# Performance work log

Hardware: AMD Instinct MI355X
Metric: run time of the kernel (lower is better)

The kernel has to match this reference:

```python
import jax, jax.numpy as jnp
import numpy as np

H, D = 16, 64  # num_heads, head_dim (hidden = H*D = 1024)
EPS = 1e-6

def elu_plus_one(x):
    return jax.nn.elu(x) + 1.0

def setup_inputs() -> dict:
    key = jax.random.key(0)
    ks = jax.random.split(key, 12)
    hid = H * D
    s = 0.02
    return {
        "hidden_states": jax.random.normal(ks[0], (1, 2048, hid), jnp.float32),
        "w_q": jax.random.normal(ks[1], (hid, hid), jnp.float32) * s,
        "w_k": jax.random.normal(ks[2], (hid, hid), jnp.float32) * s,
        "w_v": jax.random.normal(ks[3], (hid, hid), jnp.float32) * s,
        "w_o": jax.random.normal(ks[4], (hid, hid), jnp.float32) * s,
        "memory_gate": jnp.zeros((H,), jnp.float32),
        "eg_w1": jax.random.normal(ks[5], (hid, hid // 4), jnp.float32) * s,
        "eg_b1": jnp.zeros((hid // 4,), jnp.float32),
        "eg_w2": jax.random.normal(ks[6], (hid // 4, 1), jnp.float32) * s,
        "eg_b2": jnp.zeros((1,), jnp.float32),
        "fine_mem": jax.random.normal(ks[7], (4, H, D, D), jnp.float32) * s,
        "fine_norm": jax.random.uniform(ks[8], (4, H, D), jnp.float32),
    }

def _retrieve(sigma_q, memory, memory_norm):
    # sigma_q: [b,h,s,d], memory: [h,d,e], memory_norm: [h,d]
    a = jnp.einsum('bhsd,hde->bhse', sigma_q, memory)
    relevance = jnp.einsum('bhsd,hd->bhs', sigma_q, memory_norm)
    out = a / jnp.clip(relevance, EPS, None)[..., None]
    return out, relevance

def reference(hidden_states, w_q, w_k, w_v, w_o, memory_gate,
              eg_w1, eg_b1, eg_w2, eg_b2, fine_mem, fine_norm):
    B, S, hid = hidden_states.shape
    def proj(w):
        return (hidden_states @ w).reshape(B, S, H, D).transpose(0, 2, 1, 3)  # [b,h,s,d]
    q, k, v = proj(w_q), proj(w_k), proj(w_v)
    sigma_q = elu_plus_one(q)

    # coarse memory = sum of fine memories
    M_coarse = fine_mem.sum(0)        # [h,d,d]
    z_coarse = fine_norm.sum(0)       # [h,d]
    output_coarse, _ = _retrieve(sigma_q, M_coarse, z_coarse)  # [b,h,s,d]

    # learned expansion gate on coarse representation
    coarse_repr = output_coarse.transpose(0, 2, 1, 3).reshape(B, S, hid)
    logit = jax.nn.relu(coarse_repr @ eg_w1 + eg_b1) @ eg_w2 + eg_b2  # [b,s,1]
    expansion_prob = jax.nn.sigmoid(logit)                            # [b,s,1]

    # fine-grained retrieval: attention-weighted mix over the 4 banks
    outs = jnp.einsum('bhsd,fhde->fbhse', sigma_q, fine_mem)   # [f,b,h,s,d]
    rels = jnp.einsum('bhsd,fhd->fbhs', sigma_q, fine_norm)    # [f,b,h,s]
    outs = outs / jnp.clip(rels, EPS, None)[..., None]
    weights = jax.nn.softmax(rels.mean(-1), axis=0)            # [f,b,h]
    output_fine = (outs * weights[:, :, :, None, None]).sum(0)  # [b,h,s,d]

    ep = expansion_prob.transpose(0, 2, 1)[..., None]          # [b,1,s,1]
    memory_output = ep * output_fine + (1.0 - ep) * output_coarse

    # causal linear attention within current segment
    sigma_k = elu_plus_one(k)
    kv = jnp.einsum('bhsd,bhse->bhsde', sigma_k, v)            # [b,h,s,d,d]
    kv_cumsum = jnp.cumsum(kv, axis=2)
    k_cumsum = jnp.cumsum(sigma_k, axis=2)
    num = jnp.einsum('bhsd,bhsde->bhse', sigma_q, kv_cumsum)
    den = jnp.clip(jnp.einsum('bhsd,bhsd->bhs', sigma_q, k_cumsum), EPS, None)[..., None]
    local_output = num / den

    gate = jax.nn.sigmoid(memory_gate).reshape(1, H, 1, 1)
    output = gate * memory_output + (1.0 - gate) * local_output
    output = output.transpose(0, 2, 1, 3).reshape(B, S, hid)
    return output @ w_o
```

## Files before the change

### kernel.cpp

```cpp
#include <hip/hip_runtime.h>
#include <cmath>

#define EPSF 1e-6f
#define LDK 72


typedef __attribute__((ext_vector_type(8))) short bf16x8;
typedef __attribute__((ext_vector_type(4))) float f32x4;
typedef __attribute__((ext_vector_type(8))) unsigned short u16x8;

__device__ __forceinline__ float wave_allsum(float v) {
#pragma unroll
  for (int off = 32; off > 0; off >>= 1) v += __shfl_xor(v, off, 64);
  return v;
}

__device__ __forceinline__ unsigned short f2bf(float f) {
  unsigned int u = __float_as_uint(f);
  unsigned int r = (u + 0x7fffu + ((u >> 16) & 1u)) >> 16;
  return (unsigned short)r;
}
__device__ __forceinline__ float bf2f(unsigned short u) {
  return __uint_as_float(((unsigned int)u) << 16);
}

__global__ __launch_bounds__(256) void prep_kernel(const float* __restrict__ FM,
    const float* __restrict__ FN, const float* __restrict__ HS,
    const float* __restrict__ W0, const float* __restrict__ W1,
    const float* __restrict__ W2, const float* __restrict__ W3,
    const float* __restrict__ EGW1,
    unsigned short* __restrict__ MCT, float* __restrict__ ZC,
    unsigned short* __restrict__ T0, unsigned short* __restrict__ T1,
    unsigned short* __restrict__ T2, unsigned short* __restrict__ T3,
    unsigned short* __restrict__ W1T, unsigned short* __restrict__ FMT,
    unsigned short* __restrict__ HSB)
{
  int b = blockIdx.x, tid = threadIdx.x;
  __shared__ float tile[64][65];
  if (b < 64) {
    int h = b >> 2, q = b & 3;
    for (int i = tid; i < 1024; i += 256) {
      int dpl = i >> 6, e = i & 63;
      int idx = (q * 16 + dpl) * 64 + e;
      tile[dpl][e] = FM[(0 * 16 + h) * 4096 + idx] + FM[(1 * 16 + h) * 4096 + idx]
                   + FM[(2 * 16 + h) * 4096 + idx] + FM[(3 * 16 + h) * 4096 + idx];
    }
    if (q == 0 && tid < 64)
      ZC[h * 64 + tid] = FN[h * 64 + tid] + FN[1024 + h * 64 + tid]
                       + FN[2048 + h * 64 + tid] + FN[3072 + h * 64 + tid];
    __syncthreads();
    for (int i = tid; i < 1024; i += 256) {
      int e = i >> 4, dpl = i & 15;
      MCT[h * 4096 + e * 64 + q * 16 + dpl] = f2bf(tile[dpl][e]);
    }
  } else if (b < 1088) {
    int r0 = b - 64, z = r0 >> 8, rem = r0 & 255;
    const float* W = (z == 0) ? W0 : (z == 1) ? W1 : (z == 2) ? W2 : W3;
    unsigned short* WT = (z == 0) ? T0 : (z == 1) ? T1 : (z == 2) ? T2 : T3;
    int n0 = (rem & 15) * 64, k0 = (rem >> 4) * 64;
    for (int i = tid; i < 4096; i += 256) {
      int r = i >> 6, c = i & 63;
      tile[r][c] = W[(k0 + r) * 1024 + n0 + c];
    }
    __syncthreads();
    for (int i = tid; i < 1024; i += 256) {
      int r = i >> 4, c4 = (i & 15) * 4;
      ushort4 o;
      o.x = f2bf(tile[c4 + 0][r]); o.y = f2bf(tile[c4 + 1][r]);
      o.z = f2bf(tile[c4 + 2][r]); o.w = f2bf(tile[c4 + 3][r]);
      *reinterpret_cast<ushort4*>(&WT[(n0 + r) * 1024 + k0 + c4]) = o;
    }
  } else if (b < 1152) {
    int rem = b - 1088;
    int n0 = (rem & 3) * 64, k0 = (rem >> 2) * 64;
    for (int i = tid; i < 4096; i += 256) {
      int r = i >> 6, c = i & 63;
      tile[r][c] = EGW1[(k0 + r) * 256 + n0 + c];
    }
    __syncthreads();
    for (int i = tid; i < 1024; i += 256) {
      int r = i >> 4, c4 = (i & 15) * 4;
      ushort4 o;
      o.x = f2bf(tile[c4 + 0][r]); o.y = f2bf(tile[c4 + 1][r]);
      o.z = f2bf(tile[c4 + 2][r]); o.w = f2bf(tile[c4 + 3][r]);
      *reinterpret_cast<ushort4*>(&W1T[(n0 + r) * 1024 + k0 + c4]) = o;
    }
  } else if (b < 1216) {
    int mat = b - 1152;
    const float* src = FM + mat * 4096;
    for (int i = tid; i < 4096; i += 256) tile[i >> 6][i & 63] = src[i];
    __syncthreads();
    unsigned short* dst = FMT + mat * 4096;
    for (int i = tid; i < 4096; i += 256) {
      int e = i >> 6, dp = i & 63;
      dst[e * 64 + dp] = f2bf(tile[dp][e]);
    }
  } else {
    int i = (b - 1216) * 256 + tid;
    float4 v = *reinterpret_cast<const float4*>(HS + i * 4);
    ushort4 o; o.x = f2bf(v.x); o.y = f2bf(v.y); o.z = f2bf(v.z); o.w = f2bf(v.w);
    *reinterpret_cast<ushort4*>(HSB + i * 4) = o;
  }
}

__global__ __launch_bounds__(256) void mm_bf16(const unsigned short* __restrict__ A,
    const unsigned short* __restrict__ BT, float* __restrict__ C, int ldc, int act)
{
  __shared__ unsigned short As[128 * LDK];
  __shared__ unsigned short Bs[128 * LDK];
  int tid = threadIdx.x;
  int m0 = blockIdx.y * 128, n0 = blockIdx.x * 128;
  int wid = tid >> 6, lane = tid & 63;
  int wr = wid >> 1, wc = wid & 1;
  int lr = lane & 15, lg = lane >> 4;

  f32x4 acc[4][4];
#pragma unroll
  for (int m = 0; m < 4; ++m)
#pragma unroll
    for (int n = 0; n < 4; ++n)
#pragma unroll
      for (int r = 0; r < 4; ++r) acc[m][n][r] = 0.f;

  for (int kt = 0; kt < 16; ++kt) {
    int k0 = kt * 64;
#pragma unroll
    for (int p = 0; p < 4; ++p) {
      int c = p * 256 + tid;
      int row = c >> 3, k8 = c & 7;
      u16x8 va = *reinterpret_cast<const u16x8*>(A + (m0 + row) * 1024 + k0 + k8 * 8);
      *reinterpret_cast<u16x8*>(&As[row * LDK + k8 * 8]) = va;
      u16x8 vb = *reinterpret_cast<const u16x8*>(BT + (n0 + row) * 1024 + k0 + k8 * 8);
      *reinterpret_cast<u16x8*>(&Bs[row * LDK + k8 * 8]) = vb;
    }
    __syncthreads();
#pragma unroll
    for (int kk = 0; kk < 2; ++kk) {
      bf16x8 af[4], bfr[4];
#pragma unroll
      for (int m = 0; m < 4; ++m)
        af[m] = *reinterpret_cast<const bf16x8*>(&As[(wr * 64 + m * 16 + lr) * LDK + kk * 32 + lg * 8]);
#pragma unroll
      for (int n = 0; n < 4; ++n)
        bfr[n] = *reinterpret_cast<const bf16x8*>(&Bs[(wc * 64 + n * 16 + lr) * LDK + kk * 32 + lg * 8]);
#pragma unroll
      for (int m = 0; m < 4; ++m)
#pragma unroll
        for (int n = 0; n < 4; ++n)
          acc[m][n] = __builtin_amdgcn_mfma_f32_16x16x32_bf16(af[m], bfr[n], acc[m][n], 0, 0, 0);
    }
    __syncthreads();
  }
#pragma unroll
  for (int m = 0; m < 4; ++m)
#pragma unroll
    for (int n = 0; n < 4; ++n)
#pragma unroll
      for (int r = 0; r < 4; ++r) {
        float v = acc[m][n][r];
        if (act) v = v > 0.f ? v + 1.f : expf(v);
        C[(m0 + wr * 64 + m * 16 + lg * 4 + r) * ldc + n0 + wc * 64 + n * 16 + lr] = v;
      }
}

__global__ __launch_bounds__(256) void mm_gate_bf16(const unsigned short* __restrict__ MOB,
    const unsigned short* __restrict__ LOB, const float* __restrict__ MG,
    const unsigned short* __restrict__ BT, float* __restrict__ C)
{
  __shared__ unsigned short As[128 * LDK];
  __shared__ unsigned short Bs[128 * LDK];
  __shared__ float gs[16];
  int tid = threadIdx.x;
  int m0 = blockIdx.y * 128, n0 = blockIdx.x * 128;
  int wid = tid >> 6, lane = tid & 63;
  int wr = wid >> 1, wc = wid & 1;
  int lr = lane & 15, lg = lane >> 4;
  if (tid < 16) gs[tid] = 1.f / (1.f + expf(-MG[tid]));
  __syncthreads();

  f32x4 acc[4][4];
#pragma unroll
  for (int m = 0; m < 4; ++m)
#pragma unroll
    for (int n = 0; n < 4; ++n)
#pragma unroll
      for (int r = 0; r < 4; ++r) acc[m][n][r] = 0.f;

  for (int kt = 0; kt < 16; ++kt) {
    int k0 = kt * 64;
#pragma unroll
    for (int p = 0; p < 4; ++p) {
      int c = p * 256 + tid;
      int row = c >> 3, k8 = c & 7;
      int col = k0 + k8 * 8;
      float g = gs[col >> 6];
      u16x8 mv = *reinterpret_cast<const u16x8*>(MOB + (m0 + row) * 1024 + col);
      u16x8 lv = *reinterpret_cast<const u16x8*>(LOB + (m0 + row) * 1024 + col);
      u16x8 o;
#pragma unroll
      for (int j = 0; j < 8; ++j)
        o[j] = f2bf(g * bf2f((unsigned short)mv[j]) + (1.f - g) * bf2f((unsigned short)lv[j]));
      *reinterpret_cast<u16x8*>(&As[row * LDK + k8 * 8]) = o;
      u16x8 vb = *reinterpret_cast<const u16x8*>(BT + (n0 + row) * 1024 + k0 + k8 * 8);
      *reinterpret_cast<u16x8*>(&Bs[row * LDK + k8 * 8]) = vb;
    }
    __syncthreads();
#pragma unroll
    for (int kk = 0; kk < 2; ++kk) {
      bf16x8 af[4], bfr[4];
#pragma unroll
      for (int m = 0; m < 4; ++m)
        af[m] = *reinterpret_cast<const bf16x8*>(&As[(wr * 64 + m * 16 + lr) * LDK + kk * 32 + lg * 8]);
#pragma unroll
      for (int n = 0; n < 4; ++n)
        bfr[n] = *reinterpret_cast<const bf16x8*>(&Bs[(wc * 64 + n * 16 + lr) * LDK + kk * 32 + lg * 8]);
#pragma unroll
      for (int m = 0; m < 4; ++m)
#pragma unroll
        for (int n = 0; n < 4; ++n)
          acc[m][n] = __builtin_amdgcn_mfma_f32_16x16x32_bf16(af[m], bfr[n], acc[m][n], 0, 0, 0);
    }
    __syncthreads();
  }
#pragma unroll
  for (int m = 0; m < 4; ++m)
#pragma unroll
    for (int n = 0; n < 4; ++n)
#pragma unroll
      for (int r = 0; r < 4; ++r)
        C[(m0 + wr * 64 + m * 16 + lg * 4 + r) * 1024 + n0 + wc * 64 + n * 16 + lr] = acc[m][n][r];
}

__global__ __launch_bounds__(256) void proj_bf16(const unsigned short* __restrict__ A,
    const unsigned short* __restrict__ WqT, const unsigned short* __restrict__ WkT,
    const unsigned short* __restrict__ WvT,
    unsigned short* __restrict__ Oq, unsigned short* __restrict__ Ok,
    unsigned short* __restrict__ Ov)
{
  int z = blockIdx.z;
  const unsigned short* BT = (z == 0) ? WqT : (z == 1) ? WkT : WvT;
  unsigned short* C = (z == 0) ? Oq : (z == 1) ? Ok : Ov;

  __shared__ unsigned short As[128 * LDK];
  __shared__ unsigned short Bs[128 * LDK];
  int tid = threadIdx.x;
  int m0 = blockIdx.y * 128, n0 = blockIdx.x * 128;
  int wid = tid >> 6, lane = tid & 63;
  int wr = wid >> 1, wc = wid & 1;
  int lr = lane & 15, lg = lane >> 4;
  int act = (z < 2) ? 1 : 0;

  f32x4 acc[4][4];
#pragma unroll
  for (int m = 0; m < 4; ++m)
#pragma unroll
    for (int n = 0; n < 4; ++n)
#pragma unroll
      for (int r = 0; r < 4; ++r) acc[m][n][r] = 0.f;

  for (int kt = 0; kt < 16; ++kt) {
    int k0 = kt * 64;
#pragma unroll
    for (int p = 0; p < 4; ++p) {
      int c = p * 256 + tid;
      int row = c >> 3, k8 = c & 7;
      u16x8 va = *reinterpret_cast<const u16x8*>(A + (m0 + row) * 1024 + k0 + k8 * 8);
      *reinterpret_cast<u16x8*>(&As[row * LDK + k8 * 8]) = va;
      u16x8 vb = *reinterpret_cast<const u16x8*>(BT + (n0 + row) * 1024 + k0 + k8 * 8);
      *reinterpret_cast<u16x8*>(&Bs[row * LDK + k8 * 8]) = vb;
    }
    __syncthreads();
#pragma unroll
    for (int kk = 0; kk < 2; ++kk) {
      bf16x8 af[4], bfr[4];
#pragma unroll
      for (int m = 0; m < 4; ++m)
        af[m] = *reinterpret_cast<const bf16x8*>(&As[(wr * 64 + m * 16 + lr) * LDK + kk * 32 + lg * 8]);
#pragma unroll
      for (int n = 0; n < 4; ++n)
        bfr[n] = *reinterpret_cast<const bf16x8*>(&Bs[(wc * 64 + n * 16 + lr) * LDK + kk * 32 + lg * 8]);
#pragma unroll
      for (int m = 0; m < 4; ++m)
#pragma unroll
        for (int n = 0; n < 4; ++n)
          acc[m][n] = __builtin_amdgcn_mfma_f32_16x16x32_bf16(af[m], bfr[n], acc[m][n], 0, 0, 0);
    }
    __syncthreads();
  }
#pragma unroll
  for (int m = 0; m < 4; ++m)
#pragma unroll
    for (int n = 0; n < 4; ++n)
#pragma unroll
      for (int r = 0; r < 4; ++r) {
        float v = acc[m][n][r];
        if (act) v = v > 0.f ? v + 1.f : expf(v);
        C[(m0 + wr * 64 + m * 16 + lg * 4 + r) * 1024 + n0 + wc * 64 + n * 16 + lr] = f2bf(v);
      }
}

__global__ __launch_bounds__(256) void eg_fin(const float* __restrict__ H1,
    const float* __restrict__ B1, const float* __restrict__ W2,
    const float* __restrict__ B2, float* __restrict__ EP)
{
  int wid = threadIdx.x >> 6, lane = threadIdx.x & 63;
  int s = blockIdx.x * 4 + wid;
  float4 h = *reinterpret_cast<const float4*>(H1 + s * 256 + lane * 4);
  float4 b = *reinterpret_cast<const float4*>(B1 + lane * 4);
  float4 w = *reinterpret_cast<const float4*>(W2 + lane * 4);
  float v = fmaxf(h.x + b.x, 0.f) * w.x + fmaxf(h.y + b.y, 0.f) * w.y
          + fmaxf(h.z + b.z, 0.f) * w.z + fmaxf(h.w + b.w, 0.f) * w.w;
  v = wave_allsum(v);
  if (lane == 0) EP[s] = 1.f / (1.f + expf(-(v + B2[0])));
}

__global__ __launch_bounds__(256) void rels_kernel(const unsigned short* __restrict__ SQB,
    const float* __restrict__ ZC, const float* __restrict__ FN,
    float* __restrict__ RELC, float* __restrict__ RELS, float* __restrict__ PARTS)
{
  int h = blockIdx.x, st = blockIdx.y, tid = threadIdx.x;
  int s0 = st * 64;
  __shared__ float sqT[64][68];
  __shared__ float zf[5][64];
  __shared__ float relb[5][64];
#pragma unroll
  for (int p = 0; p < 2; ++p) {
    int cidx = p * 256 + tid;
    int r = cidx >> 3, d8 = cidx & 7;
    u16x8 v = *reinterpret_cast<const u16x8*>(SQB + (s0 + r) * 1024 + h * 64 + d8 * 8);
#pragma unroll
    for (int j = 0; j < 8; ++j) sqT[d8 * 8 + j][r] = bf2f((unsigned short)v[j]);
  }
  for (int idx = tid; idx < 320; idx += 256) {
    int w = idx >> 6, d = idx & 63;
    zf[w][d] = (w == 0) ? ZC[h * 64 + d] : FN[(w - 1) * 1024 + h * 64 + d];
  }
  __syncthreads();
  {
    int s = tid & 63, wh = tid >> 6;
    float r = 0.f;
    for (int dp = 0; dp < 64; ++dp) r += sqT[dp][s] * zf[wh][dp];
    relb[wh][s] = r;
    if (wh == 0) {
      float r4 = 0.f;
      for (int dp = 0; dp < 64; ++dp) r4 += sqT[dp][s] * zf[4][dp];
      relb[4][s] = r4;
    }
  }
  __syncthreads();
  if (tid < 64) {
    RELC[h * 2048 + s0 + tid] = relb[0][tid];
#pragma unroll
    for (int f = 0; f < 4; ++f)
      RELS[f * 32768 + h * 2048 + s0 + tid] = relb[1 + f][tid];
#pragma unroll
    for (int f = 0; f < 4; ++f) {
      float v = wave_allsum(relb[1 + f][tid]);
      if (tid == 0) PARTS[f * 512 + h * 32 + st] = v;
    }
  }
}

__global__ __launch_bounds__(256) void coarse_mfma(const unsigned short* __restrict__ SQB,
    const unsigned short* __restrict__ MCT, const float* __restrict__ RELC,
    unsigned short* __restrict__ COB)
{
  int h = blockIdx.x, st = blockIdx.y, tid = threadIdx.x;
  int w = tid >> 6, lane = tid & 63, lr = lane & 15, lg = lane >> 4;
  int s0 = st * 128;
  __shared__ unsigned short A_lds[128 * LDK];
  __shared__ unsigned short B_lds[64 * LDK];
#pragma unroll
  for (int p = 0; p < 4; ++p) {
    int c = p * 256 + tid;
    int row = c >> 3, k8 = c & 7;
    *reinterpret_cast<u16x8*>(&A_lds[row * LDK + k8 * 8]) =
        *reinterpret_cast<const u16x8*>(SQB + (s0 + row) * 1024 + h * 64 + k8 * 8);
  }
#pragma unroll
  for (int p = 0; p < 2; ++p) {
    int c = p * 256 + tid;
    int e = c >> 3, k8 = c & 7;
    *reinterpret_cast<u16x8*>(&B_lds[e * LDK + k8 * 8]) =
        *reinterpret_cast<const u16x8*>(MCT + h * 4096 + e * 64 + k8 * 8);
  }
  __syncthreads();

  f32x4 acc[2][4];
#pragma unroll
  for (int m = 0; m < 2; ++m)
#pragma unroll
    for (int n = 0; n < 4; ++n)
#pragma unroll
      for (int r = 0; r < 4; ++r) acc[m][n][r] = 0.f;

#pragma unroll
  for (int kk = 0; kk < 2; ++kk) {
    bf16x8 af[2], bfr[4];
#pragma unroll
    for (int m = 0; m < 2; ++m)
      af[m] = *reinterpret_cast<const bf16x8*>(&A_lds[(w * 32 + m * 16 + lr) * LDK + kk * 32 + lg * 8]);
#pragma unroll
    for (int n = 0; n < 4; ++n)
      bfr[n] = *reinterpret_cast<const bf16x8*>(&B_lds[(n * 16 + lr) * LDK + kk * 32 + lg * 8]);
#pragma unroll
    for (int m = 0; m < 2; ++m)
#pragma unroll
      for (int n = 0; n < 4; ++n)
        acc[m][n] = __builtin_amdgcn_mfma_f32_16x16x32_bf16(af[m], bfr[n], acc[m][n], 0, 0, 0);
  }
#pragma unroll
  for (int m = 0; m < 2; ++m)
#pragma unroll
    for (int r = 0; r < 4; ++r) {
      int s = s0 + w * 32 + m * 16 + lg * 4 + r;
      float rc = fmaxf(RELC[h * 2048 + s], EPSF);
#pragma unroll
      for (int n = 0; n < 4; ++n)
        COB[s * 1024 + h * 64 + n * 16 + lr] = f2bf(acc[m][n][r] / rc);
    }
}

__global__ __launch_bounds__(256) void fine_mfma(const unsigned short* __restrict__ SQB,
    const unsigned short* __restrict__ FMT, const float* __restrict__ RELS,
    const float* __restrict__ PARTS, const float* __restrict__ EP,
    const unsigned short* __restrict__ COB, unsigned short* __restrict__ MOB)
{
  int h = blockIdx.x, st = blockIdx.y;
  int tid = threadIdx.x;
  int w = tid >> 6, lane = tid & 63;
  int lr = lane & 15, lg = lane >> 4;
  int s0 = st * 128;

  __shared__ unsigned short A_lds[128 * LDK];
  __shared__ unsigned short B_lds[4 * 64 * LDK];
  __shared__ float rmean[4];
  if (tid < 4) {
    float s = 0.f;
    for (int t = 0; t < 32; ++t) s += PARTS[tid * 512 + h * 32 + t];
    rmean[tid] = s * (1.f / 2048.f);
  }

#pragma unroll
  for (int p = 0; p < 4; ++p) {
    int c = p * 256 + tid;
    int row = c >> 3, k8 = c & 7;
    *reinterpret_cast<u16x8*>(&A_lds[row * LDK + k8 * 8]) =
        *reinterpret_cast<const u16x8*>(SQB + (s0 + row) * 1024 + h * 64 + k8 * 8);
  }
#pragma unroll
  for (int p = 0; p < 8; ++p) {
    int c = p * 256 + tid;
    int f = c >> 9, rem = c & 511;
    int e = rem >> 3, k8 = rem & 7;
    *reinterpret_cast<u16x8*>(&B_lds[(f * 64 + e) * LDK + k8 * 8]) =
        *reinterpret_cast<const u16x8*>(FMT + (f * 16 + h) * 4096 + e * 64 + k8 * 8);
  }
  __syncthreads();

  f32x4 acc[4][2][4];
#pragma unroll
  for (int f = 0; f < 4; ++f)
#pragma unroll
    for (int m = 0; m < 2; ++m)
#pragma unroll
      for (int n = 0; n < 4; ++n)
#pragma unroll
        for (int r = 0; r < 4; ++r) acc[f][m][n][r] = 0.f;

#pragma unroll
  for (int kk = 0; kk < 2; ++kk) {
    bf16x8 af[2];
#pragma unroll
    for (int m = 0; m < 2; ++m)
      af[m] = *reinterpret_cast<const bf16x8*>(&A_lds[(w * 32 + m * 16 + lr) * LDK + kk * 32 + lg * 8]);
#pragma unroll
    for (int f = 0; f < 4; ++f) {
      bf16x8 bf4[4];
#pragma unroll
      for (int n = 0; n < 4; ++n)
        bf4[n] = *reinterpret_cast<const bf16x8*>(&B_lds[(f * 64 + n * 16 + lr) * LDK + kk * 32 + lg * 8]);
#pragma unroll
      for (int m = 0; m < 2; ++m)
#pragma unroll
        for (int n = 0; n < 4; ++n)
          acc[f][m][n] = __builtin_amdgcn_mfma_f32_16x16x32_bf16(af[m], bf4[n], acc[f][m][n], 0, 0, 0);
    }
  }

  float rm = fmaxf(fmaxf(rmean[0], rmean[1]), fmaxf(rmean[2], rmean[3]));
  float e0 = expf(rmean[0] - rm), e1 = expf(rmean[1] - rm);
  float e2 = expf(rmean[2] - rm), e3 = expf(rmean[3] - rm);
  float winv = 1.f / (e0 + e1 + e2 + e3);
  float w0 = e0 * winv, w1 = e1 * winv, w2 = e2 * winv, w3 = e3 * winv;

#pragma unroll
  for (int m = 0; m < 2; ++m)
#pragma unroll
    for (int r = 0; r < 4; ++r) {
      int s = s0 + w * 32 + m * 16 + lg * 4 + r;
      float e = EP[s];
      float i0 = w0 / fmaxf(RELS[0 * 32768 + h * 2048 + s], EPSF);
      float i1 = w1 / fmaxf(RELS[1 * 32768 + h * 2048 + s], EPSF);
      float i2 = w2 / fmaxf(RELS[2 * 32768 + h * 2048 + s], EPSF);
      float i3 = w3 / fmaxf(RELS[3 * 32768 + h * 2048 + s], EPSF);
#pragma unroll
      for (int n = 0; n < 4; ++n) {
        int dg = h * 64 + n * 16 + lr;
        float fine = acc[0][m][n][r] * i0 + acc[1][m][n][r] * i1
                   + acc[2][m][n][r] * i2 + acc[3][m][n][r] * i3;
        float cv = bf2f(COB[s * 1024 + dg]);
        MOB[s * 1024 + dg] = f2bf(e * fine + (1.f - e) * cv);
      }
    }
}

__global__ __launch_bounds__(256) void chunk_mfma(const unsigned short* __restrict__ SKB,
    const unsigned short* __restrict__ VVB, float* __restrict__ ST)
{
  int h = blockIdx.x, c = blockIdx.y, tid = threadIdx.x;
  int w = tid >> 6, lane = tid & 63, lr = lane & 15, lg = lane >> 4;
  int sb = c * 64;
  __shared__ unsigned short A_lds[64 * LDK];
  __shared__ unsigned short B_lds[80 * LDK];
#pragma unroll
  for (int p = 0; p < 2; ++p) {
    int cc = p * 256 + tid;
    int t = cc >> 3, e8 = cc & 7;
    u16x8 kv = *reinterpret_cast<const u16x8*>(SKB + (sb + t) * 1024 + h * 64 + e8 * 8);
    u16x8 vv = *reinterpret_cast<const u16x8*>(VVB + (sb + t) * 1024 + h * 64 + e8 * 8);
#pragma unroll
    for (int j = 0; j < 8; ++j) {
      A_lds[(e8 * 8 + j) * LDK + t] = (unsigned short)kv[j];
      B_lds[(e8 * 8 + j) * LDK + t] = (unsigned short)vv[j];
    }
  }
  if (tid < 64) B_lds[64 * LDK + tid] = 0x3F80;
  for (int i = tid; i < 15 * 64; i += 256) {
    int row = 65 + (i >> 6), col = i & 63;
    B_lds[row * LDK + col] = 0;
  }
  __syncthreads();

  f32x4 acc[5];
#pragma unroll
  for (int n = 0; n < 5; ++n)
#pragma unroll
    for (int r = 0; r < 4; ++r) acc[n][r] = 0.f;
#pragma unroll
  for (int kk = 0; kk < 2; ++kk) {
    bf16x8 af = *reinterpret_cast<const bf16x8*>(&A_lds[(w * 16 + lr) * LDK + kk * 32 + lg * 8]);
#pragma unroll
    for (int n = 0; n < 5; ++n) {
      bf16x8 bfr = *reinterpret_cast<const bf16x8*>(&B_lds[(n * 16 + lr) * LDK + kk * 32 + lg * 8]);
      acc[n] = __builtin_amdgcn_mfma_f32_16x16x32_bf16(af, bfr, acc[n], 0, 0, 0);
    }
  }
  float* base = ST + (h * 32 + c) * 4160;
#pragma unroll
  for (int r = 0; r < 4; ++r) {
    int d = w * 16 + lg * 4 + r;
#pragma unroll
    for (int n = 0; n < 4; ++n)
      base[d * 64 + n * 16 + lr] = acc[n][r];
    if (lr == 0) base[4096 + d] = acc[4][r];
  }
}

__global__ __launch_bounds__(256) void scan_kernel(const float* __restrict__ ST,
    unsigned short* __restrict__ STB)
{
  int gidx = blockIdx.x * 256 + threadIdx.x;
  int h = gidx / 4160, idx = gidx - h * 4160;
  if (h >= 16) return;
  float run = 0.f;
#pragma unroll 4
  for (int c = 0; c < 32; ++c) {
    float t = ST[(h * 32 + c) * 4160 + idx];
    STB[(h * 32 + c) * 4160 + idx] = f2bf(run);
    run += t;
  }
}

__global__ __launch_bounds__(256) void lattn_mfma(const unsigned short* __restrict__ SQB,
    const unsigned short* __restrict__ SKB, const unsigned short* __restrict__ VVB,
    const unsigned short* __restrict__ STB, unsigned short* __restrict__ LOB)
{
  int h = blockIdx.x, c = blockIdx.y, tid = threadIdx.x;
  int w = tid >> 6, lane = tid & 63, lr = lane & 15, lg = lane >> 4;
  int sb = c * 64;
  const unsigned short* stb = STB + (h * 32 + c) * 4160;

  __shared__ unsigned short A_lds[64 * LDK];
  __shared__ unsigned short K_lds[64 * LDK];
  __shared__ unsigned short P_lds[80 * LDK];
  __shared__ unsigned short V_lds[80 * LDK];
  __shared__ unsigned short S_lds[64 * LDK];

#pragma unroll
  for (int p = 0; p < 2; ++p) {
    int cc = p * 256 + tid;
    int row = cc >> 3, k8 = cc & 7;
    *reinterpret_cast<u16x8*>(&A_lds[row * LDK + k8 * 8]) =
        *reinterpret_cast<const u16x8*>(SQB + (sb + row) * 1024 + h * 64 + k8 * 8);
    *reinterpret_cast<u16x8*>(&K_lds[row * LDK + k8 * 8]) =
        *reinterpret_cast<const u16x8*>(SKB + (sb + row) * 1024 + h * 64 + k8 * 8);
  }
  for (int i = tid; i < 4096; i += 256) {
    int d = i >> 6, e = i & 63;
    P_lds[e * LDK + d] = stb[i];
  }
#pragma unroll
  for (int p = 0; p < 2; ++p) {
    int cc = p * 256 + tid;
    int t = cc >> 3, e8 = cc & 7;
    u16x8 v = *reinterpret_cast<const u16x8*>(VVB + (sb + t) * 1024 + h * 64 + e8 * 8);
#pragma unroll
    for (int j = 0; j < 8; ++j) V_lds[(e8 * 8 + j) * LDK + t] = (unsigned short)v[j];
  }
  if (tid < 64) {
    P_lds[64 * LDK + tid] = stb[4096 + tid];
    V_lds[64 * LDK + tid] = 0x3F80;
  }
  for (int i = tid; i < 15 * 64; i += 256) {
    int row = 65 + (i >> 6), col = i & 63;
    P_lds[row * LDK + col] = 0;
    V_lds[row * LDK + col] = 0;
  }
  __syncthreads();

  f32x4 acc_i[5];
#pragma unroll
  for (int n = 0; n < 5; ++n)
#pragma unroll
    for (int r = 0; r < 4; ++r) acc_i[n][r] = 0.f;
#pragma unroll
  for (int kk = 0; kk < 2; ++kk) {
    bf16x8 af = *reinterpret_cast<const bf16x8*>(&A_lds[(w * 16 + lr) * LDK + kk * 32 + lg * 8]);
#pragma unroll
    for (int n = 0; n < 5; ++n) {
      bf16x8 bfr = *reinterpret_cast<const bf16x8*>(&P_lds[(n * 16 + lr) * LDK + kk * 32 + lg * 8]);
      acc_i[n] = __builtin_amdgcn_mfma_f32_16x16x32_bf16(af, bfr, acc_i[n], 0, 0, 0);
    }
  }
  f32x4 acc_s[4];
#pragma unroll
  for (int n = 0; n < 4; ++n)
#pragma unroll
    for (int r = 0; r < 4; ++r) acc_s[n][r] = 0.f;
#pragma unroll
  for (int kk = 0; kk < 2; ++kk) {
    bf16x8 af = *reinterpret_cast<const bf16x8*>(&A_lds[(w * 16 + lr) * LDK + kk * 32 + lg * 8]);
#pragma unroll
    for (int n = 0; n < 4; ++n) {
      bf16x8 bfr = *reinterpret_cast<const bf16x8*>(&K_lds[(n * 16 + lr) * LDK + kk * 32 + lg * 8]);
      acc_s[n] = __builtin_amdgcn_mfma_f32_16x16x32_bf16(af, bfr, acc_s[n], 0, 0, 0);
    }
  }
#pragma unroll
  for (int n = 0; n < 4; ++n)
#pragma unroll
    for (int r = 0; r < 4; ++r) {
      int s_loc = w * 16 + lg * 4 + r, t = n * 16 + lr;
      float v = (t <= s_loc) ? acc_s[n][r] : 0.f;
      S_lds[s_loc * LDK + t] = f2bf(v);
    }
  __syncthreads();
  f32x4 acc_p[5];
#pragma unroll
  for (int n = 0; n < 5; ++n)
#pragma unroll
    for (int r = 0; r < 4; ++r) acc_p[n][r] = 0.f;
#pragma unroll
  for (int kk = 0; kk < 2; ++kk) {
    bf16x8 af = *reinterpret_cast<const bf16x8*>(&S_lds[(w * 16 + lr) * LDK + kk * 32 + lg * 8]);
#pragma unroll
    for (int n = 0; n < 5; ++n) {
      bf16x8 bfr = *reinterpret_cast<const bf16x8*>(&V_lds[(n * 16 + lr) * LDK + kk * 32 + lg * 8]);
      acc_p[n] = __builtin_amdgcn_mfma_f32_16x16x32_bf16(af, bfr, acc_p[n], 0, 0, 0);
    }
  }
#pragma unroll
  for (int r = 0; r < 4; ++r) {
    float den = acc_i[4][r] + acc_p[4][r];
    den = __shfl(den, lane & 48);
    den = fmaxf(den, EPSF);
    int s = sb + w * 16 + lg * 4 + r;
#pragma unroll
    for (int n = 0; n < 4; ++n)
      LOB[s * 1024 + h * 64 + n * 16 + lr] = f2bf((acc_i[n][r] + acc_p[n][r]) / den);
  }
}

extern "C" void kernel_launch(void* const* d_in, const int* in_sizes, int n_in,
                              void* d_out, int out_size, void* d_ws, size_t ws_size,
                              hipStream_t stream)
{
  const float* hs   = (const float*)d_in[0];
  const float* wq   = (const float*)d_in[1];
  const float* wk   = (const float*)d_in[2];
  const float* wv   = (const float*)d_in[3];
  const float* wo   = (const float*)d_in[4];
  const float* mg   = (const float*)d_in[5];
  const float* egw1 = (const float*)d_in[6];
  const float* egb1 = (const float*)d_in[7];
  const float* egw2 = (const float*)d_in[8];
  const float* egb2 = (const float*)d_in[9];
  const float* fm   = (const float*)d_in[10];
  const float* fn   = (const float*)d_in[11];
  float* out = (float*)d_out;

  float* ws     = (float*)d_ws;
  float* zc     = ws;
  float* rels   = zc + 1024;
  float* parts  = rels + 131072;
  float* ep     = parts + 2048;
  float* relc   = ep + 2048;
  float* states = relc + 32768;
  float* h1     = states + 2129920;
  unsigned short* hsb  = (unsigned short*)(h1 + 524288);
  unsigned short* sqb  = hsb + 2097152;
  unsigned short* skb  = sqb + 2097152;
  unsigned short* vvb  = skb + 2097152;
  unsigned short* cob  = vvb + 2097152;
  unsigned short* mob  = cob + 2097152;
  unsigned short* lob  = mob + 2097152;
  unsigned short* wqT  = lob + 2097152;
  unsigned short* wkT  = wqT + 1048576;
  unsigned short* wvT  = wkT + 1048576;
  unsigned short* woT  = wvT + 1048576;
  unsigned short* w1T  = woT + 1048576;
  unsigned short* fmbT = w1T + 262144;
  unsigned short* mcT  = fmbT + 262144;
  unsigned short* statesb = mcT + 65536;

  prep_kernel<<<3264, 256, 0, stream>>>(fm, fn, hs, wq, wk, wv, wo, egw1,
      mcT, zc, wqT, wkT, wvT, woT, w1T, fmbT, hsb);
  proj_bf16<<<dim3(8, 16, 3), 256, 0, stream>>>(hsb, wqT, wkT, wvT, sqb, skb, vvb);
  rels_kernel<<<dim3(16, 32), 256, 0, stream>>>(sqb, zc, fn, relc, rels, parts);
  coarse_mfma<<<dim3(16, 16), 256, 0, stream>>>(sqb, mcT, relc, cob);
  mm_bf16<<<dim3(2, 16), 256, 0, stream>>>(cob, w1T, h1, 256, 0);
  eg_fin<<<512, 256, 0, stream>>>(h1, egb1, egw2, egb2, ep);
  fine_mfma<<<dim3(16, 16), 256, 0, stream>>>(sqb, fmbT, rels, parts, ep, cob, mob);
  chunk_mfma<<<dim3(16, 32), 256, 0, stream>>>(skb, vvb, states);
  scan_kernel<<<260, 256, 0, stream>>>(states, statesb);
  lattn_mfma<<<dim3(16, 32), 256, 0, stream>>>(sqb, skb, vvb, statesb, lob);
  mm_gate_bf16<<<dim3(8, 16), 256, 0, stream>>>(mob, lob, mg, woT, out);
}
```

Baseline: 127.2 us.

## Merge independent memory and linear-attention stages into combined horizontal-fusion launches

Independent stages that used to be separate launches now share kernels, with the work chosen by block index: relevance with chunk states, coarse retrieval with the state scan, and local attention with the gate's first GEMM. This cuts the launch count from 11 to 8 and lets small, under-filled grids run side by side on the device. In exchange, the fused kernels reserve the larger of the two shared-memory footprints, which may lower occupancy, and blocks of different cost now run in the same grid.

```diff
diff --git a/kernel.cpp b/kernel.cpp
--- a/kernel.cpp
+++ b/kernel.cpp
@@ -103,9 +103,16 @@
   }
 }
 
-__global__ __launch_bounds__(256) void mm_bf16(const unsigned short* __restrict__ A,
-    const unsigned short* __restrict__ BT, float* __restrict__ C, int ldc, int act)
-{
+__global__ __launch_bounds__(256) void proj_bf16(const unsigned short* __restrict__ A,
+    const unsigned short* __restrict__ WqT, const unsigned short* __restrict__ WkT,
+    const unsigned short* __restrict__ WvT,
+    unsigned short* __restrict__ Oq, unsigned short* __restrict__ Ok,
+    unsigned short* __restrict__ Ov)
+{
+  int z = blockIdx.z;
+  const unsigned short* BT = (z == 0) ? WqT : (z == 1) ? WkT : WvT;
+  unsigned short* C = (z == 0) ? Oq : (z == 1) ? Ok : Ov;
+
   __shared__ unsigned short As[128 * LDK];
   __shared__ unsigned short Bs[128 * LDK];
   int tid = threadIdx.x;
@@ -113,6 +120,7 @@
   int wid = tid >> 6, lane = tid & 63;
   int wr = wid >> 1, wc = wid & 1;
   int lr = lane & 15, lg = lane >> 4;
+  int act = (z < 2) ? 1 : 0;
 
   f32x4 acc[4][4];
 #pragma unroll
@@ -159,8 +167,463 @@
       for (int r = 0; r < 4; ++r) {
         float v = acc[m][n][r];
         if (act) v = v > 0.f ? v + 1.f : expf(v);
-        C[(m0 + wr * 64 + m * 16 + lg * 4 + r) * ldc + n0 + wc * 64 + n * 16 + lr] = v;
-      }
+        C[(m0 + wr * 64 + m * 16 + lg * 4 + r) * 1024 + n0 + wc * 64 + n * 16 + lr] = f2bf(v);
+      }
+}
+
+__global__ __launch_bounds__(256) void mid1_kernel(const unsigned short* __restrict__ SQB,
+    const float* __restrict__ ZC, const float* __restrict__ FN,
+    const unsigned short* __restrict__ SKB, const unsigned short* __restrict__ VVB,
+    float* __restrict__ RELC, float* __restrict__ RELS, float* __restrict__ PARTS,
+    float* __restrict__ ST)
+{
+  __shared__ __align__(16) char smem[20736];
+  int b = blockIdx.x, tid = threadIdx.x;
+  if (b < 512) {
+    int h = b >> 5, st = b & 31;
+    int s0 = st * 64;
+    float (*sqT)[68] = (float(*)[68])smem;
+    float (*zf)[64]  = (float(*)[64])(smem + 17408);
+    float (*relb)[64]= (float(*)[64])(smem + 18688);
+#pragma unroll
+    for (int p = 0; p < 2; ++p) {
+      int cidx = p * 256 + tid;
+      int r = cidx >> 3, d8 = cidx & 7;
+      u16x8 v = *reinterpret_cast<const u16x8*>(SQB + (s0 + r) * 1024 + h * 64 + d8 * 8);
+#pragma unroll
+      for (int j = 0; j < 8; ++j) sqT[d8 * 8 + j][r] = bf2f((unsigned short)v[j]);
+    }
+    for (int idx = tid; idx < 320; idx += 256) {
+      int w = idx >> 6, d = idx & 63;
+      zf[w][d] = (w == 0) ? ZC[h * 64 + d] : FN[(w - 1) * 1024 + h * 64 + d];
+    }
+    __syncthreads();
+    {
+      int s = tid & 63, wh = tid >> 6;
+      float r = 0.f;
+      for (int dp = 0; dp < 64; ++dp) r += sqT[dp][s] * zf[wh][dp];
+      relb[wh][s] = r;
+      if (wh == 0) {
+        float r4 = 0.f;
+        for (int dp = 0; dp < 64; ++dp) r4 += sqT[dp][s] * zf[4][dp];
+        relb[4][s] = r4;
+      }
+    }
+    __syncthreads();
+    if (tid < 64) {
+      RELC[h * 2048 + s0 + tid] = relb[0][tid];
+#pragma unroll
+      for (int f = 0; f < 4; ++f)
+        RELS[f * 32768 + h * 2048 + s0 + tid] = relb[1 + f][tid];
+#pragma unroll
+      for (int f = 0; f < 4; ++f) {
+        float v = wave_allsum(relb[1 + f][tid]);
+        if (tid == 0) PARTS[f * 512 + h * 32 + st] = v;
+      }
+    }
+  } else {
+    int bb = b - 512;
+    int h = bb >> 5, c = bb & 31;
+    int w = tid >> 6, lane = tid & 63, lr = lane & 15, lg = lane >> 4;
+    int sb = c * 64;
+    unsigned short* A_lds = (unsigned short*)smem;
+    unsigned short* B_lds = (unsigned short*)(smem + 9216);
+#pragma unroll
+    for (int p = 0; p < 2; ++p) {
+      int cc = p * 256 + tid;
+      int t = cc >> 3, e8 = cc & 7;
+      u16x8 kv = *reinterpret_cast<const u16x8*>(SKB + (sb + t) * 1024 + h * 64 + e8 * 8);
+      u16x8 vv = *reinterpret_cast<const u16x8*>(VVB + (sb + t) * 1024 + h * 64 + e8 * 8);
+#pragma unroll
+      for (int j = 0; j < 8; ++j) {
+        A_lds[(e8 * 8 + j) * LDK + t] = (unsigned short)kv[j];
+        B_lds[(e8 * 8 + j) * LDK + t] = (unsigned short)vv[j];
+      }
+    }
+    if (tid < 64) B_lds[64 * LDK + tid] = 0x3F80;
+    for (int i = tid; i < 15 * 64; i += 256) {
+      int row = 65 + (i >> 6), col = i & 63;
+      B_lds[row * LDK + col] = 0;
+    }
+    __syncthreads();
+
+    f32x4 acc[5];
+#pragma unroll
+    for (int n = 0; n < 5; ++n)
+#pragma unroll
+      for (int r = 0; r < 4; ++r) acc[n][r] = 0.f;
+#pragma unroll
+    for (int kk = 0; kk < 2; ++kk) {
+      bf16x8 af = *reinterpret_cast<const bf16x8*>(&A_lds[(w * 16 + lr) * LDK + kk * 32 + lg * 8]);
+#pragma unroll
+      for (int n = 0; n < 5; ++n) {
+        bf16x8 bfr = *reinterpret_cast<const bf16x8*>(&B_lds[(n * 16 + lr) * LDK + kk * 32 + lg * 8]);
+        acc[n] = __builtin_amdgcn_mfma_f32_16x16x32_bf16(af, bfr, acc[n], 0, 0, 0);
+      }
+    }
+    float* base = ST + (h * 32 + c) * 4160;
+#pragma unroll
+    for (int r = 0; r < 4; ++r) {
+      int d = w * 16 + lg * 4 + r;
+#pragma unroll
+      for (int n = 0; n < 4; ++n)
+        base[d * 64 + n * 16 + lr] = acc[n][r];
+      if (lr == 0) base[4096 + d] = acc[4][r];
+    }
+  }
+}
+
+__global__ __launch_bounds__(256) void mid2_kernel(const unsigned short* __restrict__ SQB,
+    const unsigned short* __restrict__ MCT, const float* __restrict__ RELC,
+    const float* __restrict__ ST,
+    unsigned short* __restrict__ COB, unsigned short* __restrict__ STB)
+{
+  __shared__ __align__(16) char smem[27648];
+  int b = blockIdx.x, tid = threadIdx.x;
+  if (b < 256) {
+    int h = b >> 4, st = b & 15;
+    int w = tid >> 6, lane = tid & 63, lr = lane & 15, lg = lane >> 4;
+    int s0 = st * 128;
+    unsigned short* A_lds = (unsigned short*)smem;
+    unsigned short* B_lds = (unsigned short*)(smem + 18432);
+#pragma unroll
+    for (int p = 0; p < 4; ++p) {
+      int c = p * 256 + tid;
+      int row = c >> 3, k8 = c & 7;
+      *reinterpret_cast<u16x8*>(&A_lds[row * LDK + k8 * 8]) =
+          *reinterpret_cast<const u16x8*>(SQB + (s0 + row) * 1024 + h * 64 + k8 * 8);
+    }
+#pragma unroll
+    for (int p = 0; p < 2; ++p) {
+      int c = p * 256 + tid;
+      int e = c >> 3, k8 = c & 7;
+      *reinterpret_cast<u16x8*>(&B_lds[e * LDK + k8 * 8]) =
+          *reinterpret_cast<const u16x8*>(MCT + h * 4096 + e * 64 + k8 * 8);
+    }
+    __syncthreads();
+
+    f32x4 acc[2][4];
+#pragma unroll
+    for (int m = 0; m < 2; ++m)
+#pragma unroll
+      for (int n = 0; n < 4; ++n)
+#pragma unroll
+        for (int r = 0; r < 4; ++r) acc[m][n][r] = 0.f;
+
+#pragma unroll
+    for (int kk = 0; kk < 2; ++kk) {
+      bf16x8 af[2], bfr[4];
+#pragma unroll
+      for (int m = 0; m < 2; ++m)
+        af[m] = *reinterpret_cast<const bf16x8*>(&A_lds[(w * 32 + m * 16 + lr) * LDK + kk * 32 + lg * 8]);
+#pragma unroll
+      for (int n = 0; n < 4; ++n)
+        bfr[n] = *reinterpret_cast<const bf16x8*>(&B_lds[(n * 16 + lr) * LDK + kk * 32 + lg * 8]);
+#pragma unroll
+      for (int m = 0; m < 2; ++m)
+#pragma unroll
+        for (int n = 0; n < 4; ++n)
+          acc[m][n] = __builtin_amdgcn_mfma_f32_16x16x32_bf16(af[m], bfr[n], acc[m][n], 0, 0, 0);
+    }
+#pragma unroll
+    for (int m = 0; m < 2; ++m)
+#pragma unroll
+      for (int r = 0; r < 4; ++r) {
+        int s = s0 + w * 32 + m * 16 + lg * 4 + r;
+        float rc = fmaxf(RELC[h * 2048 + s], EPSF);
+#pragma unroll
+        for (int n = 0; n < 4; ++n)
+          COB[s * 1024 + h * 64 + n * 16 + lr] = f2bf(acc[m][n][r] / rc);
+      }
+  } else {
+    int gidx = (b - 256) * 256 + tid;
+    int h = gidx / 4160, idx = gidx - h * 4160;
+    if (h >= 16) return;
+    float run = 0.f;
+#pragma unroll 4
+    for (int c = 0; c < 32; ++c) {
+      float t = ST[(h * 32 + c) * 4160 + idx];
+      STB[(h * 32 + c) * 4160 + idx] = f2bf(run);
+      run += t;
+    }
+  }
+}
+
+__global__ __launch_bounds__(256) void mid3_kernel(const unsigned short* __restrict__ SQB,
+    const unsigned short* __restrict__ SKB, const unsigned short* __restrict__ VVB,
+    const unsigned short* __restrict__ STB, const unsigned short* __restrict__ COB,
+    const unsigned short* __restrict__ W1T,
+    unsigned short* __restrict__ LOB, float* __restrict__ H1)
+{
+  __shared__ __align__(16) char smem[50688];
+  int b = blockIdx.x, tid = threadIdx.x;
+  if (b < 512) {
+    int h = b >> 5, c = b & 31;
+    int w = tid >> 6, lane = tid & 63, lr = lane & 15, lg = lane >> 4;
+    int sb = c * 64;
+    const unsigned short* stb = STB + (h * 32 + c) * 4160;
+    unsigned short* A_lds = (unsigned short*)smem;
+    unsigned short* K_lds = (unsigned short*)(smem + 9216);
+    unsigned short* P_lds = (unsigned short*)(smem + 18432);
+    unsigned short* V_lds = (unsigned short*)(smem + 29952);
+    unsigned short* S_lds = (unsigned short*)(smem + 41472);
+
+#pragma unroll
+    for (int p = 0; p < 2; ++p) {
+      int cc = p * 256 + tid;
+      int row = cc >> 3, k8 = cc & 7;
+      *reinterpret_cast<u16x8*>(&A_lds[row * LDK + k8 * 8]) =
+          *reinterpret_cast<const u16x8*>(SQB + (sb + row) * 1024 + h * 64 + k8 * 8);
+      *reinterpret_cast<u16x8*>(&K_lds[row * LDK + k8 * 8]) =
+          *reinterpret_cast<const u16x8*>(SKB + (sb + row) * 1024 + h * 64 + k8 * 8);
+    }
+    for (int i = tid; i < 4096; i += 256) {
+      int d = i >> 6, e = i & 63;
+      P_lds[e * LDK + d] = stb[i];
+    }
+#pragma unroll
+    for (int p = 0; p < 2; ++p) {
+      int cc = p * 256 + tid;
+      int t = cc >> 3, e8 = cc & 7;
+      u16x8 v = *reinterpret_cast<const u16x8*>(VVB + (sb + t) * 1024 + h * 64 + e8 * 8);
+#pragma unroll
+      for (int j = 0; j < 8; ++j) V_lds[(e8 * 8 + j) * LDK + t] = (unsigned short)v[j];
+    }
+    if (tid < 64) {
+      P_lds[64 * LDK + tid] = stb[4096 + tid];
+      V_lds[64 * LDK + tid] = 0x3F80;
+    }
+    for (int i = tid; i < 15 * 64; i += 256) {
+      int row = 65 + (i >> 6), col = i & 63;
+      P_lds[row * LDK + col] = 0;
+      V_lds[row * LDK + col] = 0;
+    }
+    __syncthreads();
+
+    f32x4 acc_i[5];
+#pragma unroll
+    for (int n = 0; n < 5; ++n)
+#pragma unroll
+      for (int r = 0; r < 4; ++r) acc_i[n][r] = 0.f;
+#pragma unroll
+    for (int kk = 0; kk < 2; ++kk) {
+      bf16x8 af = *reinterpret_cast<const bf16x8*>(&A_lds[(w * 16 + lr) * LDK + kk * 32 + lg * 8]);
+#pragma unroll
+      for (int n = 0; n < 5; ++n) {
+        bf16x8 bfr = *reinterpret_cast<const bf16x8*>(&P_lds[(n * 16 + lr) * LDK + kk * 32 + lg * 8]);
+        acc_i[n] = __builtin_amdgcn_mfma_f32_16x16x32_bf16(af, bfr, acc_i[n], 0, 0, 0);
+      }
+    }
+    f32x4 acc_s[4];
+#pragma unroll
+    for (int n = 0; n < 4; ++n)
+#pragma unroll
+      for (int r = 0; r < 4; ++r) acc_s[n][r] = 0.f;
+#pragma unroll
+    for (int kk = 0; kk < 2; ++kk) {
+      bf16x8 af = *reinterpret_cast<const bf16x8*>(&A_lds[(w * 16 + lr) * LDK + kk * 32 + lg * 8]);
+#pragma unroll
+      for (int n = 0; n < 4; ++n) {
+        bf16x8 bfr = *reinterpret_cast<const bf16x8*>(&K_lds[(n * 16 + lr) * LDK + kk * 32 + lg * 8]);
+        acc_s[n] = __builtin_amdgcn_mfma_f32_16x16x32_bf16(af, bfr, acc_s[n], 0, 0, 0);
+      }
+    }
+#pragma unroll
+    for (int n = 0; n < 4; ++n)
+#pragma unroll
+      for (int r = 0; r < 4; ++r) {
+        int s_loc = w * 16 + lg * 4 + r, t = n * 16 + lr;
+        float v = (t <= s_loc) ? acc_s[n][r] : 0.f;
+        S_lds[s_loc * LDK + t] = f2bf(v);
+      }
+    __syncthreads();
+    f32x4 acc_p[5];
+#pragma unroll
+    for (int n = 0; n < 5; ++n)
+#pragma unroll
+      for (int r = 0; r < 4; ++r) acc_p[n][r] = 0.f;
+#pragma unroll
+    for (int kk = 0; kk < 2; ++kk) {
+      bf16x8 af = *reinterpret_cast<const bf16x8*>(&S_lds[(w * 16 + lr) * LDK + kk * 32 + lg * 8]);
+#pragma unroll
+      for (int n = 0; n < 5; ++n) {
+        bf16x8 bfr = *reinterpret_cast<const bf16x8*>(&V_lds[(n * 16 + lr) * LDK + kk * 32 + lg * 8]);
+        acc_p[n] = __builtin_amdgcn_mfma_f32_16x16x32_bf16(af, bfr, acc_p[n], 0, 0, 0);
+      }
+    }
+#pragma unroll
+    for (int r = 0; r < 4; ++r) {
+      float den = acc_i[4][r] + acc_p[4][r];
+      den = __shfl(den, lane & 48);
+      den = fmaxf(den, EPSF);
+      int s = sb + w * 16 + lg * 4 + r;
+#pragma unroll
+      for (int n = 0; n < 4; ++n)
+        LOB[s * 1024 + h * 64 + n * 16 + lr] = f2bf((acc_i[n][r] + acc_p[n][r]) / den);
+    }
+  } else {
+    int bb = b - 512;
+    int m0 = (bb >> 1) * 128, n0 = (bb & 1) * 128;
+    int wid = tid >> 6, lane = tid & 63;
+    int wr = wid >> 1, wc = wid & 1;
+    int lr = lane & 15, lg = lane >> 4;
+    unsigned short* As = (unsigned short*)smem;
+    unsigned short* Bs = (unsigned short*)(smem + 18432);
+
+    f32x4 acc[4][4];
+#pragma unroll
+    for (int m = 0; m < 4; ++m)
+#pragma unroll
+      for (int n = 0; n < 4; ++n)
+#pragma unroll
+        for (int r = 0; r < 4; ++r) acc[m][n][r] = 0.f;
+
+    for (int kt = 0; kt < 16; ++kt) {
+      int k0 = kt * 64;
+#pragma unroll
+      for (int p = 0; p < 4; ++p) {
+        int c = p * 256 + tid;
+        int row = c >> 3, k8 = c & 7;
+        u16x8 va = *reinterpret_cast<const u16x8*>(COB + (m0 + row) * 1024 + k0 + k8 * 8);
+        *reinterpret_cast<u16x8*>(&As[row * LDK + k8 * 8]) = va;
+        u16x8 vb = *reinterpret_cast<const u16x8*>(W1T + (n0 + row) * 1024 + k0 + k8 * 8);
+        *reinterpret_cast<u16x8*>(&Bs[row * LDK + k8 * 8]) = vb;
+      }
+      __syncthreads();
+#pragma unroll
+      for (int kk = 0; kk < 2; ++kk) {
+        bf16x8 af[4], bfr[4];
+#pragma unroll
+        for (int m = 0; m < 4; ++m)
+          af[m] = *reinterpret_cast<const bf16x8*>(&As[(wr * 64 + m * 16 + lr) * LDK + kk * 32 + lg * 8]);
+#pragma unroll
+        for (int n = 0; n < 4; ++n)
+          bfr[n] = *reinterpret_cast<const bf16x8*>(&Bs[(wc * 64 + n * 16 + lr) * LDK + kk * 32 + lg * 8]);
+#pragma unroll
+        for (int m = 0; m < 4; ++m)
+#pragma unroll
+          for (int n = 0; n < 4; ++n)
+            acc[m][n] = __builtin_amdgcn_mfma_f32_16x16x32_bf16(af[m], bfr[n], acc[m][n], 0, 0, 0);
+      }
+      __syncthreads();
+    }
+#pragma unroll
+    for (int m = 0; m < 4; ++m)
+#pragma unroll
+      for (int n = 0; n < 4; ++n)
+#pragma unroll
+        for (int r = 0; r < 4; ++r)
+          H1[(m0 + wr * 64 + m * 16 + lg * 4 + r) * 256 + n0 + wc * 64 + n * 16 + lr] = acc[m][n][r];
+  }
+}
+
+__global__ __launch_bounds__(256) void eg_fin(const float* __restrict__ H1,
+    const float* __restrict__ B1, const float* __restrict__ W2,
+    const float* __restrict__ B2, float* __restrict__ EP)
+{
+  int wid = threadIdx.x >> 6, lane = threadIdx.x & 63;
+  int s = blockIdx.x * 4 + wid;
+  float4 h = *reinterpret_cast<const float4*>(H1 + s * 256 + lane * 4);
+  float4 b = *reinterpret_cast<const float4*>(B1 + lane * 4);
+  float4 w = *reinterpret_cast<const float4*>(W2 + lane * 4);
+  float v = fmaxf(h.x + b.x, 0.f) * w.x + fmaxf(h.y + b.y, 0.f) * w.y
+          + fmaxf(h.z + b.z, 0.f) * w.z + fmaxf(h.w + b.w, 0.f) * w.w;
+  v = wave_allsum(v);
+  if (lane == 0) EP[s] = 1.f / (1.f + expf(-(v + B2[0])));
+}
+
+__global__ __launch_bounds__(256) void fine_mfma(const unsigned short* __restrict__ SQB,
+    const unsigned short* __restrict__ FMT, const float* __restrict__ RELS,
+    const float* __restrict__ PARTS, const float* __restrict__ EP,
+    const unsigned short* __restrict__ COB, unsigned short* __restrict__ MOB)
+{
+  int h = blockIdx.x, st = blockIdx.y;
+  int tid = threadIdx.x;
+  int w = tid >> 6, lane = tid & 63;
+  int lr = lane & 15, lg = lane >> 4;
+  int s0 = st * 128;
+
+  __shared__ unsigned short A_lds[128 * LDK];
+  __shared__ unsigned short B_lds[4 * 64 * LDK];
+  __shared__ float rmean[4];
+  if (tid < 4) {
+    float s = 0.f;
+    for (int t = 0; t < 32; ++t) s += PARTS[tid * 512 + h * 32 + t];
+    rmean[tid] = s * (1.f / 2048.f);
+  }
+
+#pragma unroll
+  for (int p = 0; p < 4; ++p) {
+    int c = p * 256 + tid;
+    int row = c >> 3, k8 = c & 7;
+    *reinterpret_cast<u16x8*>(&A_lds[row * LDK + k8 * 8]) =
+        *reinterpret_cast<const u16x8*>(SQB + (s0 + row) * 1024 + h * 64 + k8 * 8);
+  }
+#pragma unroll
+  for (int p = 0; p < 8; ++p) {
+    int c = p * 256 + tid;
+    int f = c >> 9, rem = c & 511;
+    int e = rem >> 3, k8 = rem & 7;
+    *reinterpret_cast<u16x8*>(&B_lds[(f * 64 + e) * LDK + k8 * 8]) =
+        *reinterpret_cast<const u16x8*>(FMT + (f * 16 + h) * 4096 + e * 64 + k8 * 8);
+  }
+  __syncthreads();
+
+  f32x4 acc[4][2][4];
+#pragma unroll
+  for (int f = 0; f < 4; ++f)
+#pragma unroll
+    for (int m = 0; m < 2; ++m)
+#pragma unroll
+      for (int n = 0; n < 4; ++n)
+#pragma unroll
+        for (int r = 0; r < 4; ++r) acc[f][m][n][r] = 0.f;
+
+#pragma unroll
+  for (int kk = 0; kk < 2; ++kk) {
+    bf16x8 af[2];
+#pragma unroll
+    for (int m = 0; m < 2; ++m)
+      af[m] = *reinterpret_cast<const bf16x8*>(&A_lds[(w * 32 + m * 16 + lr) * LDK + kk * 32 + lg * 8]);
+#pragma unroll
+    for (int f = 0; f < 4; ++f) {
+      bf16x8 bf4[4];
+#pragma unroll
+      for (int n = 0; n < 4; ++n)
+        bf4[n] = *reinterpret_cast<const bf16x8*>(&B_lds[(f * 64 + n * 16 + lr) * LDK + kk * 32 + lg * 8]);
+#pragma unroll
+      for (int m = 0; m < 2; ++m)
+#pragma unroll
+        for (int n = 0; n < 4; ++n)
+          acc[f][m][n] = __builtin_amdgcn_mfma_f32_16x16x32_bf16(af[m], bf4[n], acc[f][m][n], 0, 0, 0);
+    }
+  }
+
+  float rm = fmaxf(fmaxf(rmean[0], rmean[1]), fmaxf(rmean[2], rmean[3]));
+  float e0 = expf(rmean[0] - rm), e1 = expf(rmean[1] - rm);
+  float e2 = expf(rmean[2] - rm), e3 = expf(rmean[3] - rm);
+  float winv = 1.f / (e0 + e1 + e2 + e3);
+  float w0 = e0 * winv, w1 = e1 * winv, w2 = e2 * winv, w3 = e3 * winv;
+
+#pragma unroll
+  for (int m = 0; m < 2; ++m)
+#pragma unroll
+    for (int r = 0; r < 4; ++r) {
+      int s = s0 + w * 32 + m * 16 + lg * 4 + r;
+      float e = EP[s];
+      float i0 = w0 / fmaxf(RELS[0 * 32768 + h * 2048 + s], EPSF);
+      float i1 = w1 / fmaxf(RELS[1 * 32768 + h * 2048 + s], EPSF);
+      float i2 = w2 / fmaxf(RELS[2 * 32768 + h * 2048 + s], EPSF);
+      float i3 = w3 / fmaxf(RELS[3 * 32768 + h * 2048 + s], EPSF);
+#pragma unroll
+      for (int n = 0; n < 4; ++n) {
+        int dg = h * 64 + n * 16 + lr;
+        float fine = acc[0][m][n][r] * i0 + acc[1][m][n][r] * i1
+                   + acc[2][m][n][r] * i2 + acc[3][m][n][r] * i3;
+        float cv = bf2f(COB[s * 1024 + dg]);
+        MOB[s * 1024 + dg] = f2bf(e * fine + (1.f - e) * cv);
+      }
+    }
 }
 
 __global__ __launch_bounds__(256) void mm_gate_bf16(const unsigned short* __restrict__ MOB,
@@ -229,467 +692,6 @@
 #pragma unroll
       for (int r = 0; r < 4; ++r)
         C[(m0 + wr * 64 + m * 16 + lg * 4 + r) * 1024 + n0 + wc * 64 + n * 16 + lr] = acc[m][n][r];
-}
-
-__global__ __launch_bounds__(256) void proj_bf16(const unsigned short* __restrict__ A,
-    const unsigned short* __restrict__ WqT, const unsigned short* __restrict__ WkT,
-    const unsigned short* __restrict__ WvT,
-    unsigned short* __restrict__ Oq, unsigned short* __restrict__ Ok,
-    unsigned short* __restrict__ Ov)
-{
-  int z = blockIdx.z;
-  const unsigned short* BT = (z == 0) ? WqT : (z == 1) ? WkT : WvT;
-  unsigned short* C = (z == 0) ? Oq : (z == 1) ? Ok : Ov;
-
-  __shared__ unsigned short As[128 * LDK];
-  __shared__ unsigned short Bs[128 * LDK];
-  int tid = threadIdx.x;
-  int m0 = blockIdx.y * 128, n0 = blockIdx.x * 128;
-  int wid = tid >> 6, lane = tid & 63;
-  int wr = wid >> 1, wc = wid & 1;
-  int lr = lane & 15, lg = lane >> 4;
-  int act = (z < 2) ? 1 : 0;
-
-  f32x4 acc[4][4];
-#pragma unroll
-  for (int m = 0; m < 4; ++m)
-#pragma unroll
-    for (int n = 0; n < 4; ++n)
-#pragma unroll
-      for (int r = 0; r < 4; ++r) acc[m][n][r] = 0.f;
-
-  for (int kt = 0; kt < 16; ++kt) {
-    int k0 = kt * 64;
-#pragma unroll
-    for (int p = 0; p < 4; ++p) {
-      int c = p * 256 + tid;
-      int row = c >> 3, k8 = c & 7;
-      u16x8 va = *reinterpret_cast<const u16x8*>(A + (m0 + row) * 1024 + k0 + k8 * 8);
-      *reinterpret_cast<u16x8*>(&As[row * LDK + k8 * 8]) = va;
-      u16x8 vb = *reinterpret_cast<const u16x8*>(BT + (n0 + row) * 1024 + k0 + k8 * 8);
-      *reinterpret_cast<u16x8*>(&Bs[row * LDK + k8 * 8]) = vb;
-    }
-    __syncthreads();
-#pragma unroll
-    for (int kk = 0; kk < 2; ++kk) {
-      bf16x8 af[4], bfr[4];
-#pragma unroll
-      for (int m = 0; m < 4; ++m)
-        af[m] = *reinterpret_cast<const bf16x8*>(&As[(wr * 64 + m * 16 + lr) * LDK + kk * 32 + lg * 8]);
-#pragma unroll
-      for (int n = 0; n < 4; ++n)
-        bfr[n] = *reinterpret_cast<const bf16x8*>(&Bs[(wc * 64 + n * 16 + lr) * LDK + kk * 32 + lg * 8]);
-#pragma unroll
-      for (int m = 0; m < 4; ++m)
-#pragma unroll
-        for (int n = 0; n < 4; ++n)
-          acc[m][n] = __builtin_amdgcn_mfma_f32_16x16x32_bf16(af[m], bfr[n], acc[m][n], 0, 0, 0);
-    }
-    __syncthreads();
-  }
-#pragma unroll
-  for (int m = 0; m < 4; ++m)
-#pragma unroll
-    for (int n = 0; n < 4; ++n)
-#pragma unroll
-      for (int r = 0; r < 4; ++r) {
-        float v = acc[m][n][r];
-        if (act) v = v > 0.f ? v + 1.f : expf(v);
-        C[(m0 + wr * 64 + m * 16 + lg * 4 + r) * 1024 + n0 + wc * 64 + n * 16 + lr] = f2bf(v);
-      }
-}
-
-__global__ __launch_bounds__(256) void eg_fin(const float* __restrict__ H1,
-    const float* __restrict__ B1, const float* __restrict__ W2,
-    const float* __restrict__ B2, float* __restrict__ EP)
-{
-  int wid = threadIdx.x >> 6, lane = threadIdx.x & 63;
-  int s = blockIdx.x * 4 + wid;
-  float4 h = *reinterpret_cast<const float4*>(H1 + s * 256 + lane * 4);
-  float4 b = *reinterpret_cast<const float4*>(B1 + lane * 4);
-  float4 w = *reinterpret_cast<const float4*>(W2 + lane * 4);
-  float v = fmaxf(h.x + b.x, 0.f) * w.x + fmaxf(h.y + b.y, 0.f) * w.y
-          + fmaxf(h.z + b.z, 0.f) * w.z + fmaxf(h.w + b.w, 0.f) * w.w;
-  v = wave_allsum(v);
-  if (lane == 0) EP[s] = 1.f / (1.f + expf(-(v + B2[0])));
-}
-
-__global__ __launch_bounds__(256) void rels_kernel(const unsigned short* __restrict__ SQB,
-    const float* __restrict__ ZC, const float* __restrict__ FN,
-    float* __restrict__ RELC, float* __restrict__ RELS, float* __restrict__ PARTS)
-{
-  int h = blockIdx.x, st = blockIdx.y, tid = threadIdx.x;
-  int s0 = st * 64;
-  __shared__ float sqT[64][68];
-  __shared__ float zf[5][64];
-  __shared__ float relb[5][64];
-#pragma unroll
-  for (int p = 0; p < 2; ++p) {
-    int cidx = p * 256 + tid;
-    int r = cidx >> 3, d8 = cidx & 7;
-    u16x8 v = *reinterpret_cast<const u16x8*>(SQB + (s0 + r) * 1024 + h * 64 + d8 * 8);
-#pragma unroll
-    for (int j = 0; j < 8; ++j) sqT[d8 * 8 + j][r] = bf2f((unsigned short)v[j]);
-  }
-  for (int idx = tid; idx < 320; idx += 256) {
-    int w = idx >> 6, d = idx & 63;
-    zf[w][d] = (w == 0) ? ZC[h * 64 + d] : FN[(w - 1) * 1024 + h * 64 + d];
-  }
-  __syncthreads();
-  {
-    int s = tid & 63, wh = tid >> 6;
-    float r = 0.f;
-    for (int dp = 0; dp < 64; ++dp) r += sqT[dp][s] * zf[wh][dp];
-    relb[wh][s] = r;
-    if (wh == 0) {
-      float r4 = 0.f;
-      for (int dp = 0; dp < 64; ++dp) r4 += sqT[dp][s] * zf[4][dp];
-      relb[4][s] = r4;
-    }
-  }
-  __syncthreads();
-  if (tid < 64) {
-    RELC[h * 2048 + s0 + tid] = relb[0][tid];
-#pragma unroll
-    for (int f = 0; f < 4; ++f)
-      RELS[f * 32768 + h * 2048 + s0 + tid] = relb[1 + f][tid];
-#pragma unroll
-    for (int f = 0; f < 4; ++f) {
-      float v = wave_allsum(relb[1 + f][tid]);
-      if (tid == 0) PARTS[f * 512 + h * 32 + st] = v;
-    }
-  }
-}
-
-__global__ __launch_bounds__(256) void coarse_mfma(const unsigned short* __restrict__ SQB,
-    const unsigned short* __restrict__ MCT, const float* __restrict__ RELC,
-    unsigned short* __restrict__ COB)
-{
-  int h = blockIdx.x, st = blockIdx.y, tid = threadIdx.x;
-  int w = tid >> 6, lane = tid & 63, lr = lane & 15, lg = lane >> 4;
-  int s0 = st * 128;
-  __shared__ unsigned short A_lds[128 * LDK];
-  __shared__ unsigned short B_lds[64 * LDK];
-#pragma unroll
-  for (int p = 0; p < 4; ++p) {
-    int c = p * 256 + tid;
-    int row = c >> 3, k8 = c & 7;
-    *reinterpret_cast<u16x8*>(&A_lds[row * LDK + k8 * 8]) =
-        *reinterpret_cast<const u16x8*>(SQB + (s0 + row) * 1024 + h * 64 + k8 * 8);
-  }
-#pragma unroll
-  for (int p = 0; p < 2; ++p) {
-    int c = p * 256 + tid;
-    int e = c >> 3, k8 = c & 7;
-    *reinterpret_cast<u16x8*>(&B_lds[e * LDK + k8 * 8]) =
-        *reinterpret_cast<const u16x8*>(MCT + h * 4096 + e * 64 + k8 * 8);
-  }
-  __syncthreads();
-
-  f32x4 acc[2][4];
-#pragma unroll
-  for (int m = 0; m < 2; ++m)
-#pragma unroll
-    for (int n = 0; n < 4; ++n)
-#pragma unroll
-      for (int r = 0; r < 4; ++r) acc[m][n][r] = 0.f;
-
-#pragma unroll
-  for (int kk = 0; kk < 2; ++kk) {
-    bf16x8 af[2], bfr[4];
-#pragma unroll
-    for (int m = 0; m < 2; ++m)
-      af[m] = *reinterpret_cast<const bf16x8*>(&A_lds[(w * 32 + m * 16 + lr) * LDK + kk * 32 + lg * 8]);
-#pragma unroll
-    for (int n = 0; n < 4; ++n)
-      bfr[n] = *reinterpret_cast<const bf16x8*>(&B_lds[(n * 16 + lr) * LDK + kk * 32 + lg * 8]);
-#pragma unroll
-    for (int m = 0; m < 2; ++m)
-#pragma unroll
-      for (int n = 0; n < 4; ++n)
-        acc[m][n] = __builtin_amdgcn_mfma_f32_16x16x32_bf16(af[m], bfr[n], acc[m][n], 0, 0, 0);
-  }
-#pragma unroll
-  for (int m = 0; m < 2; ++m)
-#pragma unroll
-    for (int r = 0; r < 4; ++r) {
-      int s = s0 + w * 32 + m * 16 + lg * 4 + r;
-      float rc = fmaxf(RELC[h * 2048 + s], EPSF);
-#pragma unroll
-      for (int n = 0; n < 4; ++n)
-        COB[s * 1024 + h * 64 + n * 16 + lr] = f2bf(acc[m][n][r] / rc);
-    }
-}
-
-__global__ __launch_bounds__(256) void fine_mfma(const unsigned short* __restrict__ SQB,
-    const unsigned short* __restrict__ FMT, const float* __restrict__ RELS,
-    const float* __restrict__ PARTS, const float* __restrict__ EP,
-    const unsigned short* __restrict__ COB, unsigned short* __restrict__ MOB)
-{
-  int h = blockIdx.x, st = blockIdx.y;
-  int tid = threadIdx.x;
-  int w = tid >> 6, lane = tid & 63;
-  int lr = lane & 15, lg = lane >> 4;
-  int s0 = st * 128;
-
-  __shared__ unsigned short A_lds[128 * LDK];
-  __shared__ unsigned short B_lds[4 * 64 * LDK];
-  __shared__ float rmean[4];
-  if (tid < 4) {
-    float s = 0.f;
-    for (int t = 0; t < 32; ++t) s += PARTS[tid * 512 + h * 32 + t];
-    rmean[tid] = s * (1.f / 2048.f);
-  }
-
-#pragma unroll
-  for (int p = 0; p < 4; ++p) {
-    int c = p * 256 + tid;
-    int row = c >> 3, k8 = c & 7;
-    *reinterpret_cast<u16x8*>(&A_lds[row * LDK + k8 * 8]) =
-        *reinterpret_cast<const u16x8*>(SQB + (s0 + row) * 1024 + h * 64 + k8 * 8);
-  }
-#pragma unroll
-  for (int p = 0; p < 8; ++p) {
-    int c = p * 256 + tid;
-    int f = c >> 9, rem = c & 511;
-    int e = rem >> 3, k8 = rem & 7;
-    *reinterpret_cast<u16x8*>(&B_lds[(f * 64 + e) * LDK + k8 * 8]) =
-        *reinterpret_cast<const u16x8*>(FMT + (f * 16 + h) * 4096 + e * 64 + k8 * 8);
-  }
-  __syncthreads();
-
-  f32x4 acc[4][2][4];
-#pragma unroll
-  for (int f = 0; f < 4; ++f)
-#pragma unroll
-    for (int m = 0; m < 2; ++m)
-#pragma unroll
-      for (int n = 0; n < 4; ++n)
-#pragma unroll
-        for (int r = 0; r < 4; ++r) acc[f][m][n][r] = 0.f;
-
-#pragma unroll
-  for (int kk = 0; kk < 2; ++kk) {
-    bf16x8 af[2];
-#pragma unroll
-    for (int m = 0; m < 2; ++m)
-      af[m] = *reinterpret_cast<const bf16x8*>(&A_lds[(w * 32 + m * 16 + lr) * LDK + kk * 32 + lg * 8]);
-#pragma unroll
-    for (int f = 0; f < 4; ++f) {
-      bf16x8 bf4[4];
-#pragma unroll
-      for (int n = 0; n < 4; ++n)
-        bf4[n] = *reinterpret_cast<const bf16x8*>(&B_lds[(f * 64 + n * 16 + lr) * LDK + kk * 32 + lg * 8]);
-#pragma unroll
-      for (int m = 0; m < 2; ++m)
-#pragma unroll
-        for (int n = 0; n < 4; ++n)
-          acc[f][m][n] = __builtin_amdgcn_mfma_f32_16x16x32_bf16(af[m], bf4[n], acc[f][m][n], 0, 0, 0);
-    }
-  }
-
-  float rm = fmaxf(fmaxf(rmean[0], rmean[1]), fmaxf(rmean[2], rmean[3]));
-  float e0 = expf(rmean[0] - rm), e1 = expf(rmean[1] - rm);
-  float e2 = expf(rmean[2] - rm), e3 = expf(rmean[3] - rm);
-  float winv = 1.f / (e0 + e1 + e2 + e3);
-  float w0 = e0 * winv, w1 = e1 * winv, w2 = e2 * winv, w3 = e3 * winv;
-
-#pragma unroll
-  for (int m = 0; m < 2; ++m)
-#pragma unroll
-    for (int r = 0; r < 4; ++r) {
-      int s = s0 + w * 32 + m * 16 + lg * 4 + r;
-      float e = EP[s];
-      float i0 = w0 / fmaxf(RELS[0 * 32768 + h * 2048 + s], EPSF);
-      float i1 = w1 / fmaxf(RELS[1 * 32768 + h * 2048 + s], EPSF);
-      float i2 = w2 / fmaxf(RELS[2 * 32768 + h * 2048 + s], EPSF);
-      float i3 = w3 / fmaxf(RELS[3 * 32768 + h * 2048 + s], EPSF);
-#pragma unroll
-      for (int n = 0; n < 4; ++n) {
-        int dg = h * 64 + n * 16 + lr;
-        float fine = acc[0][m][n][r] * i0 + acc[1][m][n][r] * i1
-                   + acc[2][m][n][r] * i2 + acc[3][m][n][r] * i3;
-        float cv = bf2f(COB[s * 1024 + dg]);
-        MOB[s * 1024 + dg] = f2bf(e * fine + (1.f - e) * cv);
-      }
-    }
-}
-
-__global__ __launch_bounds__(256) void chunk_mfma(const unsigned short* __restrict__ SKB,
-    const unsigned short* __restrict__ VVB, float* __restrict__ ST)
-{
-  int h = blockIdx.x, c = blockIdx.y, tid = threadIdx.x;
-  int w = tid >> 6, lane = tid & 63, lr = lane & 15, lg = lane >> 4;
-  int sb = c * 64;
-  __shared__ unsigned short A_lds[64 * LDK];
-  __shared__ unsigned short B_lds[80 * LDK];
-#pragma unroll
-  for (int p = 0; p < 2; ++p) {
-    int cc = p * 256 + tid;
-    int t = cc >> 3, e8 = cc & 7;
-    u16x8 kv = *reinterpret_cast<const u16x8*>(SKB + (sb + t) * 1024 + h * 64 + e8 * 8);
-    u16x8 vv = *reinterpret_cast<const u16x8*>(VVB + (sb + t) * 1024 + h * 64 + e8 * 8);
-#pragma unroll
-    for (int j = 0; j < 8; ++j) {
-      A_lds[(e8 * 8 + j) * LDK + t] = (unsigned short)kv[j];
-      B_lds[(e8 * 8 + j) * LDK + t] = (unsigned short)vv[j];
-    }
-  }
-  if (tid < 64) B_lds[64 * LDK + tid] = 0x3F80;
-  for (int i = tid; i < 15 * 64; i += 256) {
-    int row = 65 + (i >> 6), col = i & 63;
-    B_lds[row * LDK + col] = 0;
-  }
-  __syncthreads();
-
-  f32x4 acc[5];
-#pragma unroll
-  for (int n = 0; n < 5; ++n)
-#pragma unroll
-    for (int r = 0; r < 4; ++r) acc[n][r] = 0.f;
-#pragma unroll
-  for (int kk = 0; kk < 2; ++kk) {
-    bf16x8 af = *reinterpret_cast<const bf16x8*>(&A_lds[(w * 16 + lr) * LDK + kk * 32 + lg * 8]);
-#pragma unroll
-    for (int n = 0; n < 5; ++n) {
-      bf16x8 bfr = *reinterpret_cast<const bf16x8*>(&B_lds[(n * 16 + lr) * LDK + kk * 32 + lg * 8]);
-      acc[n] = __builtin_amdgcn_mfma_f32_16x16x32_bf16(af, bfr, acc[n], 0, 0, 0);
-    }
-  }
-  float* base = ST + (h * 32 + c) * 4160;
-#pragma unroll
-  for (int r = 0; r < 4; ++r) {
-    int d = w * 16 + lg * 4 + r;
-#pragma unroll
-    for (int n = 0; n < 4; ++n)
-      base[d * 64 + n * 16 + lr] = acc[n][r];
-    if (lr == 0) base[4096 + d] = acc[4][r];
-  }
-}
-
-__global__ __launch_bounds__(256) void scan_kernel(const float* __restrict__ ST,
-    unsigned short* __restrict__ STB)
-{
-  int gidx = blockIdx.x * 256 + threadIdx.x;
-  int h = gidx / 4160, idx = gidx - h * 4160;
-  if (h >= 16) return;
-  float run = 0.f;
-#pragma unroll 4
-  for (int c = 0; c < 32; ++c) {
-    float t = ST[(h * 32 + c) * 4160 + idx];
-    STB[(h * 32 + c) * 4160 + idx] = f2bf(run);
-    run += t;
-  }
-}
-
-__global__ __launch_bounds__(256) void lattn_mfma(const unsigned short* __restrict__ SQB,
-    const unsigned short* __restrict__ SKB, const unsigned short* __restrict__ VVB,
-    const unsigned short* __restrict__ STB, unsigned short* __restrict__ LOB)
-{
-  int h = blockIdx.x, c = blockIdx.y, tid = threadIdx.x;
-  int w = tid >> 6, lane = tid & 63, lr = lane & 15, lg = lane >> 4;
-  int sb = c * 64;
-  const unsigned short* stb = STB + (h * 32 + c) * 4160;
-
-  __shared__ unsigned short A_lds[64 * LDK];
-  __shared__ unsigned short K_lds[64 * LDK];
-  __shared__ unsigned short P_lds[80 * LDK];
-  __shared__ unsigned short V_lds[80 * LDK];
-  __shared__ unsigned short S_lds[64 * LDK];
-
-#pragma unroll
-  for (int p = 0; p < 2; ++p) {
-    int cc = p * 256 + tid;
-    int row = cc >> 3, k8 = cc & 7;
-    *reinterpret_cast<u16x8*>(&A_lds[row * LDK + k8 * 8]) =
-        *reinterpret_cast<const u16x8*>(SQB + (sb + row) * 1024 + h * 64 + k8 * 8);
-    *reinterpret_cast<u16x8*>(&K_lds[row * LDK + k8 * 8]) =
-        *reinterpret_cast<const u16x8*>(SKB + (sb + row) * 1024 + h * 64 + k8 * 8);
-  }
-  for (int i = tid; i < 4096; i += 256) {
-    int d = i >> 6, e = i & 63;
-    P_lds[e * LDK + d] = stb[i];
-  }
-#pragma unroll
-  for (int p = 0; p < 2; ++p) {
-    int cc = p * 256 + tid;
-    int t = cc >> 3, e8 = cc & 7;
-    u16x8 v = *reinterpret_cast<const u16x8*>(VVB + (sb + t) * 1024 + h * 64 + e8 * 8);
-#pragma unroll
-    for (int j = 0; j < 8; ++j) V_lds[(e8 * 8 + j) * LDK + t] = (unsigned short)v[j];
-  }
-  if (tid < 64) {
-    P_lds[64 * LDK + tid] = stb[4096 + tid];
-    V_lds[64 * LDK + tid] = 0x3F80;
-  }
-  for (int i = tid; i < 15 * 64; i += 256) {
-    int row = 65 + (i >> 6), col = i & 63;
-    P_lds[row * LDK + col] = 0;
-    V_lds[row * LDK + col] = 0;
-  }
-  __syncthreads();
-
-  f32x4 acc_i[5];
-#pragma unroll
-  for (int n = 0; n < 5; ++n)
-#pragma unroll
-    for (int r = 0; r < 4; ++r) acc_i[n][r] = 0.f;
-#pragma unroll
-  for (int kk = 0; kk < 2; ++kk) {
-    bf16x8 af = *reinterpret_cast<const bf16x8*>(&A_lds[(w * 16 + lr) * LDK + kk * 32 + lg * 8]);
-#pragma unroll
-    for (int n = 0; n < 5; ++n) {
-      bf16x8 bfr = *reinterpret_cast<const bf16x8*>(&P_lds[(n * 16 + lr) * LDK + kk * 32 + lg * 8]);
-      acc_i[n] = __builtin_amdgcn_mfma_f32_16x16x32_bf16(af, bfr, acc_i[n], 0, 0, 0);
-    }
-  }
-  f32x4 acc_s[4];
-#pragma unroll
-  for (int n = 0; n < 4; ++n)
-#pragma unroll
-    for (int r = 0; r < 4; ++r) acc_s[n][r] = 0.f;
-#pragma unroll
-  for (int kk = 0; kk < 2; ++kk) {
-    bf16x8 af = *reinterpret_cast<const bf16x8*>(&A_lds[(w * 16 + lr) * LDK + kk * 32 + lg * 8]);
-#pragma unroll
-    for (int n = 0; n < 4; ++n) {
-      bf16x8 bfr = *reinterpret_cast<const bf16x8*>(&K_lds[(n * 16 + lr) * LDK + kk * 32 + lg * 8]);
-      acc_s[n] = __builtin_amdgcn_mfma_f32_16x16x32_bf16(af, bfr, acc_s[n], 0, 0, 0);
-    }
-  }
-#pragma unroll
-  for (int n = 0; n < 4; ++n)
-#pragma unroll
-    for (int r = 0; r < 4; ++r) {
-      int s_loc = w * 16 + lg * 4 + r, t = n * 16 + lr;
-      float v = (t <= s_loc) ? acc_s[n][r] : 0.f;
-      S_lds[s_loc * LDK + t] = f2bf(v);
-    }
-  __syncthreads();
-  f32x4 acc_p[5];
-#pragma unroll
-  for (int n = 0; n < 5; ++n)
-#pragma unroll
-    for (int r = 0; r < 4; ++r) acc_p[n][r] = 0.f;
-#pragma unroll
-  for (int kk = 0; kk < 2; ++kk) {
-    bf16x8 af = *reinterpret_cast<const bf16x8*>(&S_lds[(w * 16 + lr) * LDK + kk * 32 + lg * 8]);
-#pragma unroll
-    for (int n = 0; n < 5; ++n) {
-      bf16x8 bfr = *reinterpret_cast<const bf16x8*>(&V_lds[(n * 16 + lr) * LDK + kk * 32 + lg * 8]);
-      acc_p[n] = __builtin_amdgcn_mfma_f32_16x16x32_bf16(af, bfr, acc_p[n], 0, 0, 0);
-    }
-  }
-#pragma unroll
-  for (int r = 0; r < 4; ++r) {
-    float den = acc_i[4][r] + acc_p[4][r];
-    den = __shfl(den, lane & 48);
-    den = fmaxf(den, EPSF);
-    int s = sb + w * 16 + lg * 4 + r;
-#pragma unroll
-    for (int n = 0; n < 4; ++n)
-      LOB[s * 1024 + h * 64 + n * 16 + lr] = f2bf((acc_i[n][r] + acc_p[n][r]) / den);
-  }
 }
 
 extern "C" void kernel_launch(void* const* d_in, const int* in_sizes, int n_in,
@@ -737,13 +739,10 @@
   prep_kernel<<<3264, 256, 0, stream>>>(fm, fn, hs, wq, wk, wv, wo, egw1,
       mcT, zc, wqT, wkT, wvT, woT, w1T, fmbT, hsb);
   proj_bf16<<<dim3(8, 16, 3), 256, 0, stream>>>(hsb, wqT, wkT, wvT, sqb, skb, vvb);
-  rels_kernel<<<dim3(16, 32), 256, 0, stream>>>(sqb, zc, fn, relc, rels, parts);
-  coarse_mfma<<<dim3(16, 16), 256, 0, stream>>>(sqb, mcT, relc, cob);
-  mm_bf16<<<dim3(2, 16), 256, 0, stream>>>(cob, w1T, h1, 256, 0);
+  mid1_kernel<<<1024, 256, 0, stream>>>(sqb, zc, fn, skb, vvb, relc, rels, parts, states);
+  mid2_kernel<<<516, 256, 0, stream>>>(sqb, mcT, relc, states, cob, statesb);
+  mid3_kernel<<<544, 256, 0, stream>>>(sqb, skb, vvb, statesb, cob, w1T, lob, h1);
   eg_fin<<<512, 256, 0, stream>>>(h1, egb1, egw2, egb2, ep);
   fine_mfma<<<dim3(16, 16), 256, 0, stream>>>(sqb, fmbT, rels, parts, ep, cob, mob);
-  chunk_mfma<<<dim3(16, 32), 256, 0, stream>>>(skb, vvb, states);
-  scan_kernel<<<260, 256, 0, stream>>>(states, statesb);
-  lattn_mfma<<<dim3(16, 32), 256, 0, stream>>>(sqb, skb, vvb, statesb, lob);
   mm_gate_bf16<<<dim3(8, 16), 256, 0, stream>>>(mob, lob, mg, woT, out);
 }
```

Result: faster. 119.6 us (median of 2 runs) (-5.9%).
